# Kernel optimization log

Hardware: AMD Instinct MI355X
Metric: run time of the kernel (lower is better)

## Reference

```python
import jax, jax.numpy as jnp
import numpy as np

H_BINS = 61
INSZ = 150
EPS = 1e-6


def rgb_uv_hist(img, sigma_u, sigma_v, c):
    """Differentiable RGB-uv soft histogram with per-channel RBF kernels.
    img: [B,3,H,W] in [0,1]; sigma_u, sigma_v, c: [3]. Returns [B,3,h,h]."""
    B = img.shape[0]
    x = jnp.clip(img, 0.0, 1.0).reshape(B, 3, -1)          # [B,3,P]
    Iy = jnp.sqrt(jnp.sum(x * x, axis=1))                  # [B,P] intensity weight
    lg = jnp.log(x + EPS)
    # log-chromaticity (u,v) per reference channel c in {R,G,B}
    u = jnp.stack([lg[:, 0] - lg[:, 1], lg[:, 1] - lg[:, 0], lg[:, 2] - lg[:, 0]], 1)  # [B,3,P]
    v = jnp.stack([lg[:, 0] - lg[:, 2], lg[:, 1] - lg[:, 2], lg[:, 2] - lg[:, 1]], 1)
    bins = jnp.linspace(-3.0, 3.0, H_BINS).astype(img.dtype)
    ku = jnp.exp(-((u[..., None] - bins) ** 2) / (sigma_u[None, :, None, None] ** 2))  # [B,3,P,h]
    kv = jnp.exp(-((v[..., None] - bins) ** 2) / (sigma_v[None, :, None, None] ** 2))
    w = Iy[:, None, :] * c[None, :, None]                  # [B,3,P]
    hist = jnp.einsum('bcpu,bcp,bcpv->bcuv', ku, w, kv)    # [B,3,h,h]
    norm = jnp.sum(hist, axis=(1, 2, 3), keepdims=True) + EPS
    return hist / norm


def _conv(x, w, b, stride):
    y = jax.lax.conv_general_dilated(x, w, (stride, stride), 'VALID',
                                     dimension_numbers=('NCHW', 'OIHW', 'NCHW'))
    return jax.nn.relu(y + b[None, :, None, None])


def _head(hist, w1, b1, w2, b2, w3, b3, fc):
    z = _conv(hist, w1, b1, 2)   # 61 -> 29
    z = _conv(z, w2, b2, 2)      # 29 -> 14
    z = _conv(z, w3, b3, 1)      # 14 -> 13
    z = z.reshape(z.shape[0], -1)  # [B, 512*13*13]
    return jnp.abs(z @ fc.T)


def setup_inputs() -> dict:
    key = jax.random.key(0)
    ks = jax.random.split(key, 16)
    B = 16
    d = {}
    d['image'] = jax.random.uniform(ks[0], (B, 3, INSZ, INSZ), jnp.float32)
    # hist params: sigmas in a numerically reasonable range (orig init: random()*0.02)
    d['su_s'] = 0.05 + 0.2 * jax.random.uniform(ks[1], (3,), jnp.float32)
    d['sv_s'] = 0.05 + 0.2 * jax.random.uniform(ks[2], (3,), jnp.float32)
    d['c_s'] = jnp.ones((3,), jnp.float32)
    d['w1_s'] = 0.05 * jax.random.normal(ks[3], (128, 3, 5, 5), jnp.float32)
    d['b1_s'] = jnp.zeros((128,), jnp.float32)
    d['w2_s'] = 0.02 * jax.random.normal(ks[4], (256, 128, 3, 3), jnp.float32)
    d['b2_s'] = jnp.zeros((256,), jnp.float32)
    d['w3_s'] = 0.02 * jax.random.normal(ks[5], (512, 256, 2, 2), jnp.float32)
    d['b3_s'] = jnp.zeros((512,), jnp.float32)
    d['fc_s'] = 0.003 * jax.random.normal(ks[6], (9, 512 * 13 * 13), jnp.float32)
    d['su_i'] = 0.05 + 0.2 * jax.random.uniform(ks[7], (3,), jnp.float32)
    d['sv_i'] = 0.05 + 0.2 * jax.random.uniform(ks[8], (3,), jnp.float32)
    d['c_i'] = jnp.ones((3,), jnp.float32)
    d['w1_i'] = 0.05 * jax.random.normal(ks[9], (128, 3, 5, 5), jnp.float32)
    d['b1_i'] = jnp.zeros((128,), jnp.float32)
    d['w2_i'] = 0.02 * jax.random.normal(ks[10], (256, 128, 3, 3), jnp.float32)
    d['b2_i'] = jnp.zeros((256,), jnp.float32)
    d['w3_i'] = 0.02 * jax.random.normal(ks[11], (512, 256, 2, 2), jnp.float32)
    d['b3_i'] = jnp.zeros((512,), jnp.float32)
    d['fc_i'] = 0.003 * jax.random.normal(ks[12], (3, 512 * 13 * 13), jnp.float32)
    return d


def reference(image, su_s, sv_s, c_s, w1_s, b1_s, w2_s, b2_s, w3_s, b3_s, fc_s,
              su_i, sv_i, c_i, w1_i, b1_i, w2_i, b2_i, w3_i, b3_i, fc_i):
    B = image.shape[0]
    # sensor branch: hist -> CNN -> |fc| -> 3x3 matrix (transposed), L1-row-norm scaled
    hs = rgb_uv_hist(image, su_s, sv_s, c_s)
    m = _head(hs, w1_s, b1_s, w2_s, b2_s, w3_s, b3_s, fc_s).reshape(B, 3, 3)
    m = jnp.swapaxes(m, -1, -2)                               # .t()
    n = jnp.max(jnp.sum(jnp.abs(m), axis=-1), axis=-1) + 1e-4  # max L1 row norm, [B]
    m = m / n[:, None, None]
    # color mapping: pixels @ m^T
    mapped = jnp.einsum('bjhw,bij->bihw', image, m)
    # illuminant branch on mapped image
    hi = rgb_uv_hist(mapped, su_i, sv_i, c_i)
    ill = _head(hi, w1_i, b1_i, w2_i, b2_i, w3_i, b3_i, fc_i)  # [B,3]
    est_ill = jnp.einsum('bij,bj->bi', jnp.linalg.inv(m), ill)
    return est_ill
```

## Files before the change

kernel.cpp:

```cpp
#include <hip/hip_runtime.h>

#define P_PIX 22500
#define HB 61
#define HSP 21
#define PPB 1152
#define NCHK 9

typedef float f32x4 __attribute__((ext_vector_type(4)));
typedef _Float16 f16x8 __attribute__((ext_vector_type(8)));
typedef _Float16 f16x4 __attribute__((ext_vector_type(4)));

__global__ __launch_bounds__(256) void hist_mfma(
    const float* __restrict__ img, const float* __restrict__ su,
    const float* __restrict__ sv, const float* __restrict__ cw,
    const float* __restrict__ msc, float* __restrict__ hpart)
{
    const int bc = blockIdx.x;
    const int b = bc / 3, c = bc % 3;
    const int split = blockIdx.y;
    const int tid  = threadIdx.x;
    const int wv   = tid >> 6;
    const int lane = tid & 63;
    const int quad = lane >> 4;
    const int mr   = lane & 15;

    __shared__ __align__(16) _Float16 B_lds[8192];
    __shared__ float suu[128], svv[128], sww[128];

    const float sig_u = su[c], sig_v = sv[c];
    const float inv_su2 = 1.f / (sig_u * sig_u);
    const float inv_sv2 = 1.f / (sig_v * sig_v);
    const float cwc = cw[c];
    const float ubin_b = -3.f + 0.1f * (float)lane;
    const float ubin_a = -3.f + 0.1f * (float)(wv * 16 + mr);

    const bool hasM = (msc != nullptr);
    float m00=0,m01=0,m02=0,m10=0,m11=0,m12=0,m20=0,m21=0,m22=0;
    if (hasM) {
        const float* mp = msc + b * 9;
        m00=mp[0]; m01=mp[1]; m02=mp[2];
        m10=mp[3]; m11=mp[4]; m12=mp[5];
        m20=mp[6]; m21=mp[7]; m22=mp[8];
    }

    const int p0   = split * PPB;
    const int pend = min(p0 + PPB, P_PIX);

    f32x4 acc[4];
#pragma unroll
    for (int nt = 0; nt < 4; ++nt) acc[nt] = (f32x4){0.f, 0.f, 0.f, 0.f};

    for (int chunk = 0; chunk < NCHK; ++chunk) {
        __syncthreads();
        if (tid < 128) {
            int px = p0 + chunk * 128 + tid;
            float u = 0.f, v = 0.f, wgt = 0.f;
            if (px < pend) {
                const float* ip = img + (size_t)b * 3 * P_PIX + px;
                float r = ip[0], g = ip[P_PIX], bl = ip[2 * P_PIX];
                if (hasM) {
                    float r2 = m00 * r + m01 * g + m02 * bl;
                    float g2 = m10 * r + m11 * g + m12 * bl;
                    float b2 = m20 * r + m21 * g + m22 * bl;
                    r = r2; g = g2; bl = b2;
                }
                r  = fminf(fmaxf(r, 0.f), 1.f);
                g  = fminf(fmaxf(g, 0.f), 1.f);
                bl = fminf(fmaxf(bl, 0.f), 1.f);
                float Iy = sqrtf(r * r + g * g + bl * bl);
                float lr = __logf(r + 1e-6f);
                float lg = __logf(g + 1e-6f);
                float lb = __logf(bl + 1e-6f);
                if (c == 0)      { u = lr - lg; v = lr - lb; }
                else if (c == 1) { u = lg - lr; v = lg - lb; }
                else             { u = lb - lr; v = lb - lg; }
                wgt = Iy * cwc;
            }
            suu[tid] = u; svv[tid] = v; sww[tid] = wgt;
        }
        __syncthreads();
#pragma unroll
        for (int r = 0; r < 4; ++r) {
            int pg = wv + 4 * r;
            f32x4 v0 = *(const f32x4*)&svv[pg * 8];
            f32x4 v1 = *(const f32x4*)&svv[pg * 8 + 4];
            f16x8 bv;
#pragma unroll
            for (int j = 0; j < 4; ++j) {
                float dv = v0[j] - ubin_b;
                bv[j] = (_Float16)__expf(-dv * dv * inv_sv2);
                float dv1 = v1[j] - ubin_b;
                bv[4 + j] = (_Float16)__expf(-dv1 * dv1 * inv_sv2);
            }
            *(f16x8*)&B_lds[(pg * 64 + lane) * 8] = bv;
        }
        f16x8 af[4];
#pragma unroll
        for (int kk = 0; kk < 4; ++kk) {
            int pxg = kk * 4 + quad;
            f32x4 u0 = *(const f32x4*)&suu[pxg * 8];
            f32x4 u1 = *(const f32x4*)&suu[pxg * 8 + 4];
            f32x4 w0 = *(const f32x4*)&sww[pxg * 8];
            f32x4 w1 = *(const f32x4*)&sww[pxg * 8 + 4];
#pragma unroll
            for (int j = 0; j < 4; ++j) {
                float du = u0[j] - ubin_a;
                af[kk][j] = (_Float16)(__expf(-du * du * inv_su2) * w0[j]);
                float du1 = u1[j] - ubin_a;
                af[kk][4 + j] = (_Float16)(__expf(-du1 * du1 * inv_su2) * w1[j]);
            }
        }
        __syncthreads();
#pragma unroll
        for (int kk = 0; kk < 4; ++kk) {
            int pgq = kk * 4 + quad;
#pragma unroll
            for (int nt = 0; nt < 4; ++nt) {
                f16x8 bvv = *(const f16x8*)&B_lds[(pgq * 64 + nt * 16 + mr) * 8];
                acc[nt] = __builtin_amdgcn_mfma_f32_16x16x32_f16(af[kk], bvv, acc[nt], 0, 0, 0);
            }
        }
    }

    float* hp = hpart + ((size_t)bc * HSP + split) * 4096;
#pragma unroll
    for (int nt = 0; nt < 4; ++nt) {
        int v = nt * 16 + mr;
#pragma unroll
        for (int r = 0; r < 4; ++r) {
            int u = wv * 16 + quad * 4 + r;
            hp[u * 64 + v] = acc[nt][r];
        }
    }
}

__global__ __launch_bounds__(256) void reduce_hist(
    const float* __restrict__ hpart, float* __restrict__ hist,
    float* __restrict__ hsum3)
{
    const int bc = blockIdx.x;
    const int part = blockIdx.y;
    const int tid = threadIdx.x;
    const float* base = hpart + (size_t)bc * HSP * 4096;
    float lsum = 0.f;
#pragma unroll
    for (int t = 0; t < 4; ++t) {
        int idx = part * 1024 + t * 256 + tid;
        int u = idx >> 6, v = idx & 63;
        float s = 0.f;
        for (int sp = 0; sp < HSP; ++sp) s += base[sp * 4096 + idx];
        if (u < HB && v < HB) {
            hist[(size_t)bc * (HB * HB) + u * HB + v] = s;
            lsum += s;
        }
    }
    __shared__ float red[4];
    for (int off = 32; off; off >>= 1) lsum += __shfl_down(lsum, off, 64);
    if ((tid & 63) == 0) red[tid >> 6] = lsum;
    __syncthreads();
    if (tid == 0) atomicAdd(&hsum3[bc], red[0] + red[1] + red[2] + red[3]);
}

__global__ __launch_bounds__(256) void conv1_mfma(
    const float* __restrict__ hist, const float* __restrict__ hsum3,
    const _Float16* __restrict__ w1h, const float* __restrict__ bias,
    _Float16* __restrict__ out)
{
    const int b    = blockIdx.x;
    const int m0   = blockIdx.y * 128;
    const int tid  = threadIdx.x;
    const int wv   = tid >> 6;
    const int lane = tid & 63;
    const int quad = lane >> 4;
    const int mr   = lane & 15;

    __shared__ __align__(16) _Float16 A_lds[128 * 96];

    const float sc = 1.f / (hsum3[b * 3] + hsum3[b * 3 + 1] + hsum3[b * 3 + 2] + 1e-6f);
    const float* inb = hist + (size_t)b * 3 * 3721;

    for (int slot = tid; slot < 1536; slot += 256) {
        int m  = slot & 127;
        int kg = slot >> 7;
        int mg = m0 + m;
        bool mok = (mg < 841);
        int oh = mok ? mg / 29 : 0;
        int ow = mok ? mg % 29 : 0;
        const float* pbase = inb + (oh * 2) * 61 + (ow * 2);
        f16x8 av;
#pragma unroll
        for (int j = 0; j < 8; ++j) {
            int k = kg * 8 + j;
            float x = 0.f;
            if (mok && k < 75) {
                int ci = k / 25, r = k % 25;
                int kh = r / 5, kw = r % 5;
                x = pbase[ci * 3721 + kh * 61 + kw] * sc;
            }
            av[j] = (_Float16)x;
        }
        *(f16x8*)&A_lds[(kg * 128 + m) * 8] = av;
    }
    __syncthreads();

    f16x8 wf[3][2];
#pragma unroll
    for (int ks = 0; ks < 3; ++ks)
#pragma unroll
        for (int nt = 0; nt < 2; ++nt) {
            int co = (wv * 2 + nt) * 16 + mr;
            wf[ks][nt] = *(const f16x8*)&w1h[co * 96 + ks * 32 + quad * 8];
        }

    f32x4 acc[8][2];
#pragma unroll
    for (int mt = 0; mt < 8; ++mt)
#pragma unroll
        for (int nt = 0; nt < 2; ++nt) acc[mt][nt] = (f32x4){0.f, 0.f, 0.f, 0.f};

#pragma unroll
    for (int ks = 0; ks < 3; ++ks)
#pragma unroll
        for (int mt = 0; mt < 8; ++mt) {
            f16x8 bv = *(const f16x8*)&A_lds[((ks * 4 + quad) * 128 + mt * 16 + mr) * 8];
#pragma unroll
            for (int nt = 0; nt < 2; ++nt)
                acc[mt][nt] = __builtin_amdgcn_mfma_f32_16x16x32_f16(bv, wf[ks][nt], acc[mt][nt], 0, 0, 0);
        }

#pragma unroll
    for (int mt = 0; mt < 8; ++mt) {
#pragma unroll
        for (int r = 0; r < 4; ++r) {
            int sp = m0 + mt * 16 + quad * 4 + r;
            if (sp >= 841) continue;
#pragma unroll
            for (int nt = 0; nt < 2; ++nt) {
                int co = (wv * 2 + nt) * 16 + mr;
                float y = acc[mt][nt][r] + bias[co];
                out[((size_t)b * 841 + sp) * 128 + co] = (_Float16)fmaxf(y, 0.f);
            }
        }
    }
}

template<int CIN, int COUT, int Kk, int S, int IN, int OUT,
         int NPB, int KSPL, int KCH>
__global__ __launch_bounds__(256) void conv_mfma(
    const _Float16* __restrict__ in_h,
    const _Float16* __restrict__ w_h,
    float* __restrict__ out)
{
    constexpr int KK   = Kk * Kk;
    constexpr int OSZ  = OUT * OUT;
    constexpr int MT   = (OSZ + 15) / 16;
    constexpr int MP   = MT * 16;
    constexpr int KTOT = CIN * KK;
    constexpr int KC   = KTOT / KSPL;
    constexpr int NCHUNK = KC / KCH;
    constexpr int NT   = NPB / 64;
    constexpr int KSN  = KCH / 32;
    constexpr int SLOTS = MP * (KCH / 8);

    const int b   = blockIdx.x;
    const int co0 = blockIdx.y * NPB;
    const int k00 = blockIdx.z * KC;
    const int tid  = threadIdx.x;
    const int wv   = tid >> 6;
    const int lane = tid & 63;
    const int quad = lane >> 4;
    const int mr   = lane & 15;

    __shared__ __align__(16) _Float16 A_lds[MP * KCH];

    const _Float16* inb = in_h + (size_t)b * (IN * IN) * CIN;
    float* outp = out + (size_t)blockIdx.z * gridDim.x * OSZ * COUT;

    f32x4 acc[MT][NT];
#pragma unroll
    for (int mt = 0; mt < MT; ++mt)
#pragma unroll
        for (int nt = 0; nt < NT; ++nt) acc[mt][nt] = (f32x4){0.f, 0.f, 0.f, 0.f};

    for (int ch = 0; ch < NCHUNK; ++ch) {
        const int k0 = k00 + ch * KCH;
        __syncthreads();
        for (int slot = tid; slot < SLOTS; slot += 256) {
            int m  = slot % MP;
            int kg = slot / MP;
            bool mok = (m < OSZ);
            int oh = mok ? m / OUT : 0;
            int ow = mok ? m % OUT : 0;
            int kbase = k0 + kg * 8;
            int khkw = kbase / CIN;
            int ci0  = kbase % CIN;
            int kh = khkw / Kk, kw = khkw % Kk;
            f16x8 av = (f16x8)(_Float16)0.f;
            if (mok)
                av = *(const f16x8*)&inb[((size_t)((oh * S + kh) * IN + (ow * S + kw))) * CIN + ci0];
            *(f16x8*)&A_lds[(kg * MP + m) * 8] = av;
        }
        __syncthreads();
        f16x8 wf[KSN][NT];
#pragma unroll
        for (int ks = 0; ks < KSN; ++ks)
#pragma unroll
            for (int nt = 0; nt < NT; ++nt) {
                int co = co0 + (wv * NT + nt) * 16 + mr;
                wf[ks][nt] = *(const f16x8*)&w_h[(size_t)co * KTOT + k0 + ks * 32 + quad * 8];
            }
#pragma unroll
        for (int ks = 0; ks < KSN; ++ks) {
#pragma unroll
            for (int mt = 0; mt < MT; ++mt) {
                f16x8 bv = *(const f16x8*)&A_lds[((ks * 4 + quad) * MP + mt * 16 + mr) * 8];
#pragma unroll
                for (int nt = 0; nt < NT; ++nt)
                    acc[mt][nt] = __builtin_amdgcn_mfma_f32_16x16x32_f16(bv, wf[ks][nt], acc[mt][nt], 0, 0, 0);
            }
        }
    }

#pragma unroll
    for (int mt = 0; mt < MT; ++mt) {
#pragma unroll
        for (int r = 0; r < 4; ++r) {
            int sp = mt * 16 + quad * 4 + r;
            if (sp >= OSZ) continue;
#pragma unroll
            for (int nt = 0; nt < NT; ++nt) {
                int co = co0 + (wv * NT + nt) * 16 + mr;
                outp[((size_t)b * OSZ + sp) * COUT + co] = acc[mt][nt][r];
            }
        }
    }
}

__global__ __launch_bounds__(256) void reduce_bias_relu_f16(
    const float* __restrict__ p, const float* __restrict__ bias,
    _Float16* __restrict__ out, int cout, int total4, int kspl, int total)
{
    for (int i4 = blockIdx.x * 256 + threadIdx.x; i4 < total4; i4 += gridDim.x * 256) {
        f32x4 s = (f32x4){0.f, 0.f, 0.f, 0.f};
        for (int ks = 0; ks < kspl; ++ks)
            s += *(const f32x4*)&p[(size_t)ks * total + i4 * 4];
        f32x4 bb = *(const f32x4*)&bias[(i4 * 4) % cout];
        f16x4 o;
#pragma unroll
        for (int j = 0; j < 4; ++j) o[j] = (_Float16)fmaxf(s[j] + bb[j], 0.f);
        *(f16x4*)&out[(size_t)i4 * 4] = o;
    }
}

__global__ __launch_bounds__(256) void fc_mfma(
    const _Float16* __restrict__ z,
    const _Float16* __restrict__ fcw,
    float* __restrict__ out, int NO)
{
    const int tid  = threadIdx.x;
    const int wv   = tid >> 6;
    const int lane = tid & 63;
    const int quad = lane >> 4;
    const int mr   = lane & 15;
    const int kw0  = blockIdx.x * 512 + wv * 128;

    __shared__ float sred[1024];

    f32x4 acc = (f32x4){0.f, 0.f, 0.f, 0.f};
    const bool bok = (mr < NO);
#pragma unroll
    for (int ks = 0; ks < 4; ++ks) {
        int kk = kw0 + ks * 32 + quad * 8;
        f16x8 av = *(const f16x8*)&z[(size_t)mr * 86528 + kk];
        f16x8 bw = (f16x8)(_Float16)0.f;
        if (bok) bw = *(const f16x8*)&fcw[(size_t)mr * 86528 + kk];
        acc = __builtin_amdgcn_mfma_f32_16x16x32_f16(av, bw, acc, 0, 0, 0);
    }
#pragma unroll
    for (int r = 0; r < 4; ++r)
        sred[wv * 256 + (quad * 4 + r) * 16 + mr] = acc[r];
    __syncthreads();
    if (tid < 256) {
        float s = sred[tid] + sred[256 + tid] + sred[512 + tid] + sred[768 + tid];
        int o = tid & 15, b = tid >> 4;
        if (o < NO) atomicAdd(&out[b * NO + o], s);
    }
}

__global__ __launch_bounds__(256) void prep_weights(
    const float* __restrict__ w1s, const float* __restrict__ w1i,
    const float* __restrict__ w2s, const float* __restrict__ w3s,
    const float* __restrict__ w2i, const float* __restrict__ w3i,
    const float* __restrict__ fcs, const float* __restrict__ fci,
    _Float16* __restrict__ w1h, _Float16* __restrict__ w23,
    _Float16* __restrict__ fch)
{
    const int R1 = 24576;
    const int N2 = 294912, N3 = 524288;
    const int R2 = 2 * (N2 + N3);
    const int K = 86528;
    const int R3 = 12 * K;
    const int T = R1 + R2 + R3;
    for (int i = blockIdx.x * 256 + threadIdx.x; i < T; i += gridDim.x * 256) {
        if (i < R1) {
            int br = i / 12288, r = i % 12288;
            int co = r / 96, k = r % 96;
            const float* s = br ? w1i : w1s;
            w1h[i] = (k < 75) ? (_Float16)s[co * 75 + k] : (_Float16)0.f;
        } else if (i < R1 + R2) {
            int j = i - R1;
            int out_idx = j;
            const float* s; int CK, KKn;
            if (j < N2)                { s = w2s; CK = 1152; KKn = 9; }
            else if (j < N2 + N3)      { s = w3s; j -= N2; CK = 1024; KKn = 4; }
            else if (j < 2 * N2 + N3)  { s = w2i; j -= N2 + N3; CK = 1152; KKn = 9; }
            else                       { s = w3i; j -= 2 * N2 + N3; CK = 1024; KKn = 4; }
            int co = j / CK, rem = j % CK;
            int ci = rem % (CK / KKn), khkw = rem / (CK / KKn);
            w23[out_idx] = (_Float16)s[co * CK + ci * KKn + khkw];
        } else {
            int j = i - R1 - R2;
            int o = j / K, rem = j % K;
            int sp = rem / 512, co = rem % 512;
            const float* s = (o < 9) ? (fcs + o * K) : (fci + (o - 9) * K);
            fch[j] = (_Float16)s[co * 169 + sp];
        }
    }
}

__global__ void build_m(const float* __restrict__ h, float* __restrict__ msc)
{
    int b = threadIdx.x;
    if (b < 16) {
        float m[9];
#pragma unroll
        for (int i = 0; i < 3; ++i)
#pragma unroll
            for (int j = 0; j < 3; ++j) m[i * 3 + j] = fabsf(h[b * 9 + j * 3 + i]);
        float n = 0.f;
#pragma unroll
        for (int i = 0; i < 3; ++i) {
            float r = m[i * 3] + m[i * 3 + 1] + m[i * 3 + 2];
            n = fmaxf(n, r);
        }
        n += 1e-4f;
        float inv = 1.f / n;
#pragma unroll
        for (int k = 0; k < 9; ++k) msc[b * 9 + k] = m[k] * inv;
    }
}

__global__ void final_est(const float* __restrict__ msc, const float* __restrict__ ill,
                          float* __restrict__ out)
{
    int bidx = threadIdx.x;
    if (bidx < 16) {
        const float* m = msc + bidx * 9;
        float a = m[0], b = m[1], c = m[2];
        float d = m[3], e = m[4], f = m[5];
        float g = m[6], h = m[7], i = m[8];
        float A = e * i - f * h, B = f * g - d * i, C = d * h - e * g;
        float D = c * h - b * i, E = a * i - c * g, F = b * g - a * h;
        float G = b * f - c * e, H = c * d - a * f, I = a * e - b * d;
        float det = a * A + b * B + c * C;
        float inv_det = 1.f / det;
        float x0 = fabsf(ill[bidx * 3 + 0]);
        float x1 = fabsf(ill[bidx * 3 + 1]);
        float x2 = fabsf(ill[bidx * 3 + 2]);
        out[bidx * 3 + 0] = (A * x0 + D * x1 + G * x2) * inv_det;
        out[bidx * 3 + 1] = (B * x0 + E * x1 + H * x2) * inv_det;
        out[bidx * 3 + 2] = (C * x0 + F * x1 + I * x2) * inv_det;
    }
}

extern "C" void kernel_launch(void* const* d_in, const int* in_sizes, int n_in,
                              void* d_out, int out_size, void* d_ws, size_t ws_size,
                              hipStream_t stream)
{
    (void)in_sizes; (void)n_in; (void)out_size; (void)ws_size;
    const float* image = (const float*)d_in[0];
    const float* su_s  = (const float*)d_in[1];
    const float* sv_s  = (const float*)d_in[2];
    const float* c_s   = (const float*)d_in[3];
    const float* w1_s  = (const float*)d_in[4];
    const float* b1_s  = (const float*)d_in[5];
    const float* w2_s  = (const float*)d_in[6];
    const float* b2_s  = (const float*)d_in[7];
    const float* w3_s  = (const float*)d_in[8];
    const float* b3_s  = (const float*)d_in[9];
    const float* fc_s  = (const float*)d_in[10];
    const float* su_i  = (const float*)d_in[11];
    const float* sv_i  = (const float*)d_in[12];
    const float* c_i   = (const float*)d_in[13];
    const float* w1_i  = (const float*)d_in[14];
    const float* b1_i  = (const float*)d_in[15];
    const float* w2_i  = (const float*)d_in[16];
    const float* b2_i  = (const float*)d_in[17];
    const float* w3_i  = (const float*)d_in[18];
    const float* b3_i  = (const float*)d_in[19];
    const float* fc_i  = (const float*)d_in[20];

    float* W     = (float*)d_ws;
    float* hist  = W;
    float* hd    = hist + 178608;
    float* hsum3 = hd + 144;
    float* msc   = hsum3 + 48;
    float* p2    = msc + 144;
    float* p3    = p2 + 3211264;
    float* hpart = p3 + 2768896;
    _Float16* o1h   = (_Float16*)(hpart + 48 * HSP * 4096);
    _Float16* o2h   = o1h   + 1722368;
    _Float16* o3h   = o2h   + 802816;
    _Float16* fch   = o3h   + 1384448;
    _Float16* w2h_s = fch   + 1038336;
    _Float16* w3h_s = w2h_s + 294912;
    _Float16* w2h_i = w3h_s + 524288;
    _Float16* w3h_i = w2h_i + 294912;
    _Float16* w1h_s = w3h_i + 524288;
    _Float16* w1h_i = w1h_s + 12288;

    const int O2_TOT = 16 * 196 * 256;
    const int O3_TOT = 16 * 169 * 512;
    const int FCK = 86528;

    prep_weights<<<1024, 256, 0, stream>>>(w1_s, w1_i, w2_s, w3_s, w2_i, w3_i,
                                           fc_s, fc_i, w1h_s, w2h_s, fch);

    hipMemsetAsync(hd, 0, 192 * 4, stream);
    hist_mfma<<<dim3(48, HSP), 256, 0, stream>>>(image, su_s, sv_s, c_s, nullptr, hpart);
    reduce_hist<<<dim3(48, 4), 256, 0, stream>>>(hpart, hist, hsum3);
    conv1_mfma<<<dim3(16, 7), 256, 0, stream>>>(hist, hsum3, w1h_s, b1_s, o1h);
    conv_mfma<128, 256, 3, 2, 29, 14, 128, 4, 96><<<dim3(16, 2, 4), 256, 0, stream>>>(o1h, w2h_s, p2);
    reduce_bias_relu_f16<<<784, 256, 0, stream>>>(p2, b2_s, o2h, 256, O2_TOT / 4, 4, O2_TOT);
    conv_mfma<256, 512, 2, 1, 14, 13, 128, 2, 64><<<dim3(16, 4, 2), 256, 0, stream>>>(o2h, w3h_s, p3);
    reduce_bias_relu_f16<<<1024, 256, 0, stream>>>(p3, b3_s, o3h, 512, O3_TOT / 4, 2, O3_TOT);
    fc_mfma<<<169, 256, 0, stream>>>(o3h, fch, hd, 9);
    build_m<<<1, 64, 0, stream>>>(hd, msc);

    hipMemsetAsync(hd, 0, 192 * 4, stream);
    hist_mfma<<<dim3(48, HSP), 256, 0, stream>>>(image, su_i, sv_i, c_i, msc, hpart);
    reduce_hist<<<dim3(48, 4), 256, 0, stream>>>(hpart, hist, hsum3);
    conv1_mfma<<<dim3(16, 7), 256, 0, stream>>>(hist, hsum3, w1h_i, b1_i, o1h);
    conv_mfma<128, 256, 3, 2, 29, 14, 128, 4, 96><<<dim3(16, 2, 4), 256, 0, stream>>>(o1h, w2h_i, p2);
    reduce_bias_relu_f16<<<784, 256, 0, stream>>>(p2, b2_i, o2h, 256, O2_TOT / 4, 4, O2_TOT);
    conv_mfma<256, 512, 2, 1, 14, 13, 128, 2, 64><<<dim3(16, 4, 2), 256, 0, stream>>>(o2h, w3h_i, p3);
    reduce_bias_relu_f16<<<1024, 256, 0, stream>>>(p3, b3_i, o3h, 512, O3_TOT / 4, 2, O3_TOT);
    fc_mfma<<<169, 256, 0, stream>>>(o3h, fch + 9 * FCK, hd, 3);
    final_est<<<1, 64, 0, stream>>>(msc, hd, (float*)d_out);
}
```

Baseline: 358.7 us.

## Raise split-K parallelism in conv kernels and fold memsets into weight prep

Halves the conv1 spatial tile so twice as many blocks run, and raises the split-K factor of conv2 from 4 to 12 and conv3 from 2 to 8 to fill more compute units. The hd zeroing moves into prep_weights, removing the two hipMemsetAsync calls; the second branch gets its own hd2 and hsum3 buffers so no re-zeroing is needed. hpart, p2 and p3 now share one aliased workspace region. The cost is more partial-sum traffic in the reduction kernels.

Measured after the change: 342.8 us. 4.4% less time.

```diff
diff --git a/kernel.cpp b/kernel.cpp
--- a/kernel.cpp
+++ b/kernel.cpp
@@ -167,21 +167,21 @@
     _Float16* __restrict__ out)
 {
     const int b    = blockIdx.x;
-    const int m0   = blockIdx.y * 128;
+    const int m0   = blockIdx.y * 64;
     const int tid  = threadIdx.x;
     const int wv   = tid >> 6;
     const int lane = tid & 63;
     const int quad = lane >> 4;
     const int mr   = lane & 15;
 
-    __shared__ __align__(16) _Float16 A_lds[128 * 96];
+    __shared__ __align__(16) _Float16 A_lds[64 * 96];
 
     const float sc = 1.f / (hsum3[b * 3] + hsum3[b * 3 + 1] + hsum3[b * 3 + 2] + 1e-6f);
     const float* inb = hist + (size_t)b * 3 * 3721;
 
-    for (int slot = tid; slot < 1536; slot += 256) {
-        int m  = slot & 127;
-        int kg = slot >> 7;
+    for (int slot = tid; slot < 768; slot += 256) {
+        int m  = slot & 63;
+        int kg = slot >> 6;
         int mg = m0 + m;
         bool mok = (mg < 841);
         int oh = mok ? mg / 29 : 0;
@@ -199,7 +199,7 @@
             }
             av[j] = (_Float16)x;
         }
-        *(f16x8*)&A_lds[(kg * 128 + m) * 8] = av;
+        *(f16x8*)&A_lds[(kg * 64 + m) * 8] = av;
     }
     __syncthreads();
 
@@ -212,24 +212,24 @@
             wf[ks][nt] = *(const f16x8*)&w1h[co * 96 + ks * 32 + quad * 8];
         }
 
-    f32x4 acc[8][2];
-#pragma unroll
-    for (int mt = 0; mt < 8; ++mt)
+    f32x4 acc[4][2];
+#pragma unroll
+    for (int mt = 0; mt < 4; ++mt)
 #pragma unroll
         for (int nt = 0; nt < 2; ++nt) acc[mt][nt] = (f32x4){0.f, 0.f, 0.f, 0.f};
 
 #pragma unroll
     for (int ks = 0; ks < 3; ++ks)
 #pragma unroll
-        for (int mt = 0; mt < 8; ++mt) {
-            f16x8 bv = *(const f16x8*)&A_lds[((ks * 4 + quad) * 128 + mt * 16 + mr) * 8];
+        for (int mt = 0; mt < 4; ++mt) {
+            f16x8 bv = *(const f16x8*)&A_lds[((ks * 4 + quad) * 64 + mt * 16 + mr) * 8];
 #pragma unroll
             for (int nt = 0; nt < 2; ++nt)
                 acc[mt][nt] = __builtin_amdgcn_mfma_f32_16x16x32_f16(bv, wf[ks][nt], acc[mt][nt], 0, 0, 0);
         }
 
 #pragma unroll
-    for (int mt = 0; mt < 8; ++mt) {
+    for (int mt = 0; mt < 4; ++mt) {
 #pragma unroll
         for (int r = 0; r < 4; ++r) {
             int sp = m0 + mt * 16 + quad * 4 + r;
@@ -393,22 +393,26 @@
     const float* __restrict__ w2i, const float* __restrict__ w3i,
     const float* __restrict__ fcs, const float* __restrict__ fci,
     _Float16* __restrict__ w1h, _Float16* __restrict__ w23,
-    _Float16* __restrict__ fch)
-{
+    _Float16* __restrict__ fch, float* __restrict__ zp)
+{
+    const int R0 = 384;
     const int R1 = 24576;
     const int N2 = 294912, N3 = 524288;
     const int R2 = 2 * (N2 + N3);
     const int K = 86528;
     const int R3 = 12 * K;
-    const int T = R1 + R2 + R3;
+    const int T = R0 + R1 + R2 + R3;
     for (int i = blockIdx.x * 256 + threadIdx.x; i < T; i += gridDim.x * 256) {
-        if (i < R1) {
-            int br = i / 12288, r = i % 12288;
+        if (i < R0) {
+            zp[i] = 0.f;
+        } else if (i < R0 + R1) {
+            int r0 = i - R0;
+            int br = r0 / 12288, r = r0 % 12288;
             int co = r / 96, k = r % 96;
             const float* s = br ? w1i : w1s;
-            w1h[i] = (k < 75) ? (_Float16)s[co * 75 + k] : (_Float16)0.f;
-        } else if (i < R1 + R2) {
-            int j = i - R1;
+            w1h[r0] = (k < 75) ? (_Float16)s[co * 75 + k] : (_Float16)0.f;
+        } else if (i < R0 + R1 + R2) {
+            int j = i - R0 - R1;
             int out_idx = j;
             const float* s; int CK, KKn;
             if (j < N2)                { s = w2s; CK = 1152; KKn = 9; }
@@ -419,7 +423,7 @@
             int ci = rem % (CK / KKn), khkw = rem / (CK / KKn);
             w23[out_idx] = (_Float16)s[co * CK + ci * KKn + khkw];
         } else {
-            int j = i - R1 - R2;
+            int j = i - R0 - R1 - R2;
             int o = j / K, rem = j % K;
             int sp = rem / 512, co = rem % 512;
             const float* s = (o < 9) ? (fcs + o * K) : (fci + (o - 9) * K);
@@ -500,15 +504,18 @@
     const float* b3_i  = (const float*)d_in[19];
     const float* fc_i  = (const float*)d_in[20];
 
-    float* W     = (float*)d_ws;
-    float* hist  = W;
-    float* hd    = hist + 178608;
-    float* hsum3 = hd + 144;
-    float* msc   = hsum3 + 48;
-    float* p2    = msc + 144;
-    float* p3    = p2 + 3211264;
-    float* hpart = p3 + 2768896;
-    _Float16* o1h   = (_Float16*)(hpart + 48 * HSP * 4096);
+    float* W      = (float*)d_ws;
+    float* hist   = W;
+    float* hd     = hist + 178608;
+    float* hd2    = hd + 144;
+    float* hsum3a = hd2 + 144;
+    float* hsum3b = hsum3a + 48;
+    float* msc    = hsum3b + 48;
+    float* U      = msc + 144;
+    float* hpart  = U;
+    float* p2     = U;
+    float* p3     = U;
+    _Float16* o1h   = (_Float16*)(U + 11075584);
     _Float16* o2h   = o1h   + 1722368;
     _Float16* o3h   = o2h   + 802816;
     _Float16* fch   = o3h   + 1384448;
@@ -524,27 +531,25 @@
     const int FCK = 86528;
 
     prep_weights<<<1024, 256, 0, stream>>>(w1_s, w1_i, w2_s, w3_s, w2_i, w3_i,
-                                           fc_s, fc_i, w1h_s, w2h_s, fch);
-
-    hipMemsetAsync(hd, 0, 192 * 4, stream);
+                                           fc_s, fc_i, w1h_s, w2h_s, fch, hd);
+
     hist_mfma<<<dim3(48, HSP), 256, 0, stream>>>(image, su_s, sv_s, c_s, nullptr, hpart);
-    reduce_hist<<<dim3(48, 4), 256, 0, stream>>>(hpart, hist, hsum3);
-    conv1_mfma<<<dim3(16, 7), 256, 0, stream>>>(hist, hsum3, w1h_s, b1_s, o1h);
-    conv_mfma<128, 256, 3, 2, 29, 14, 128, 4, 96><<<dim3(16, 2, 4), 256, 0, stream>>>(o1h, w2h_s, p2);
-    reduce_bias_relu_f16<<<784, 256, 0, stream>>>(p2, b2_s, o2h, 256, O2_TOT / 4, 4, O2_TOT);
-    conv_mfma<256, 512, 2, 1, 14, 13, 128, 2, 64><<<dim3(16, 4, 2), 256, 0, stream>>>(o2h, w3h_s, p3);
-    reduce_bias_relu_f16<<<1024, 256, 0, stream>>>(p3, b3_s, o3h, 512, O3_TOT / 4, 2, O3_TOT);
+    reduce_hist<<<dim3(48, 4), 256, 0, stream>>>(hpart, hist, hsum3a);
+    conv1_mfma<<<dim3(16, 14), 256, 0, stream>>>(hist, hsum3a, w1h_s, b1_s, o1h);
+    conv_mfma<128, 256, 3, 2, 29, 14, 128, 12, 96><<<dim3(16, 2, 12), 256, 0, stream>>>(o1h, w2h_s, p2);
+    reduce_bias_relu_f16<<<784, 256, 0, stream>>>(p2, b2_s, o2h, 256, O2_TOT / 4, 12, O2_TOT);
+    conv_mfma<256, 512, 2, 1, 14, 13, 128, 8, 64><<<dim3(16, 4, 8), 256, 0, stream>>>(o2h, w3h_s, p3);
+    reduce_bias_relu_f16<<<1024, 256, 0, stream>>>(p3, b3_s, o3h, 512, O3_TOT / 4, 8, O3_TOT);
     fc_mfma<<<169, 256, 0, stream>>>(o3h, fch, hd, 9);
     build_m<<<1, 64, 0, stream>>>(hd, msc);
 
-    hipMemsetAsync(hd, 0, 192 * 4, stream);
     hist_mfma<<<dim3(48, HSP), 256, 0, stream>>>(image, su_i, sv_i, c_i, msc, hpart);
-    reduce_hist<<<dim3(48, 4), 256, 0, stream>>>(hpart, hist, hsum3);
-    conv1_mfma<<<dim3(16, 7), 256, 0, stream>>>(hist, hsum3, w1h_i, b1_i, o1h);
-    conv_mfma<128, 256, 3, 2, 29, 14, 128, 4, 96><<<dim3(16, 2, 4), 256, 0, stream>>>(o1h, w2h_i, p2);
-    reduce_bias_relu_f16<<<784, 256, 0, stream>>>(p2, b2_i, o2h, 256, O2_TOT / 4, 4, O2_TOT);
-    conv_mfma<256, 512, 2, 1, 14, 13, 128, 2, 64><<<dim3(16, 4, 2), 256, 0, stream>>>(o2h, w3h_i, p3);
-    reduce_bias_relu_f16<<<1024, 256, 0, stream>>>(p3, b3_i, o3h, 512, O3_TOT / 4, 2, O3_TOT);
-    fc_mfma<<<169, 256, 0, stream>>>(o3h, fch + 9 * FCK, hd, 3);
-    final_est<<<1, 64, 0, stream>>>(msc, hd, (float*)d_out);
-}
+    reduce_hist<<<dim3(48, 4), 256, 0, stream>>>(hpart, hist, hsum3b);
+    conv1_mfma<<<dim3(16, 14), 256, 0, stream>>>(hist, hsum3b, w1h_i, b1_i, o1h);
+    conv_mfma<128, 256, 3, 2, 29, 14, 128, 12, 96><<<dim3(16, 2, 12), 256, 0, stream>>>(o1h, w2h_i, p2);
+    reduce_bias_relu_f16<<<784, 256, 0, stream>>>(p2, b2_i, o2h, 256, O2_TOT / 4, 12, O2_TOT);
+    conv_mfma<256, 512, 2, 1, 14, 13, 128, 8, 64><<<dim3(16, 4, 8), 256, 0, stream>>>(o2h, w3h_i, p3);
+    reduce_bias_relu_f16<<<1024, 256, 0, stream>>>(p3, b3_i, o3h, 512, O3_TOT / 4, 8, O3_TOT);
+    fc_mfma<<<169, 256, 0, stream>>>(o3h, fch + 9 * FCK, hd2, 3);
+    final_est<<<1, 64, 0, stream>>>(msc, hd2, (float*)d_out);
+}
```
